# Performance work log

Measured on AMD Instinct MI355X. Metric: run time of the kernel, lower is better.

## Reference

```python
import jax, jax.numpy as jnp
import numpy as np
import math

B, SV, ST, D, H = 16, 1024, 512, 768, 8
DH = D // H


def layernorm(x, g, b, eps=1e-5):
    m = jnp.mean(x, axis=-1, keepdims=True)
    v = jnp.var(x, axis=-1, keepdims=True)
    return (x - m) / jnp.sqrt(v + eps) * g + b


def setup_inputs() -> dict:
    key = jax.random.key(0)
    ks = jax.random.split(key, 12)
    s = 1.0 / math.sqrt(D)
    inp = {
        "visual_features": jax.random.normal(ks[0], (B, SV, D), jnp.float32),
        "text_features": jax.random.normal(ks[1], (B, ST, D), jnp.float32),
        "visual_mask": jnp.ones((B, SV), jnp.int32),
        "text_mask": jnp.ones((B, ST), jnp.int32),
        "Wq": jax.random.normal(ks[2], (D, D), jnp.float32) * s,
        "bq": jnp.zeros((D,), jnp.float32),
        "Wk": jax.random.normal(ks[3], (D, D), jnp.float32) * s,
        "bk": jnp.zeros((D,), jnp.float32),
        "Wv": jax.random.normal(ks[4], (D, D), jnp.float32) * s,
        "bv": jnp.zeros((D,), jnp.float32),
        "Wo": jax.random.normal(ks[5], (D, D), jnp.float32) * s,
        "bo": jnp.zeros((D,), jnp.float32),
        "ln1_g": jnp.ones((D,), jnp.float32),
        "ln1_b": jnp.zeros((D,), jnp.float32),
        "Wf": jax.random.normal(ks[6], (2 * D, D), jnp.float32) * (1.0 / math.sqrt(2 * D)),
        "bf": jnp.zeros((D,), jnp.float32),
        "ln2_g": jnp.ones((D,), jnp.float32),
        "ln2_b": jnp.zeros((D,), jnp.float32),
    }
    return inp


def _heads(x):
    b, s, _ = x.shape
    return x.reshape(b, s, H, DH)


def _cross_attn(q_feats, kv_feats, kv_mask, Wq, bq, Wk, bk, Wv, bv):
    # q_feats: [B,Sq,D], kv_feats: [B,Sk,D], kv_mask: [B,Sk] or None
    q = _heads(q_feats @ Wq + bq)   # [B,Sq,H,DH]
    k = _heads(kv_feats @ Wk + bk)  # [B,Sk,H,DH]
    v = _heads(kv_feats @ Wv + bv)
    scores = jnp.einsum('bqhd,bkhd->bhqk', q, k) / math.sqrt(DH)
    if kv_mask is not None:
        scores = jnp.where(kv_mask[:, None, None, :] == 0, -jnp.inf, scores)
    attn = jax.nn.softmax(scores, axis=-1)  # dropout is identity in eval
    out = jnp.einsum('bhqk,bkhd->bqhd', attn, v)
    return out.reshape(q_feats.shape[0], q_feats.shape[1], D)


def reference(visual_features, text_features, visual_mask, text_mask,
              Wq, bq, Wk, bk, Wv, bv, Wo, bo, ln1_g, ln1_b,
              Wf, bf, ln2_g, ln2_b):
    # visual queries attend to text
    v2t = _cross_attn(visual_features, text_features, text_mask, Wq, bq, Wk, bk, Wv, bv)
    # text queries attend to visual
    t2v = _cross_attn(text_features, visual_features, visual_mask, Wq, bq, Wk, bk, Wv, bv)
    attended_visual = layernorm(visual_features + (v2t @ Wo + bo), ln1_g, ln1_b)
    attended_text = layernorm(text_features + (t2v @ Wo + bo), ln1_g, ln1_b)
    # masked mean pooling
    vm = visual_mask[:, :, None].astype(jnp.float32)
    pooled_v = (attended_visual * vm).sum(1) / vm.sum(1)
    tm = text_mask[:, :, None].astype(jnp.float32)
    pooled_t = (attended_text * tm).sum(1) / tm.sum(1)
    fused = jnp.concatenate([pooled_v, pooled_t], axis=-1) @ Wf + bf
    fused = layernorm(fused, ln2_g, ln2_b)  # dropout identity in eval
    return fused
```

## Files before the change

kernel.cpp:

```cpp
#include <hip/hip_runtime.h>

typedef __bf16 bf16x8 __attribute__((ext_vector_type(8)));
typedef float f32x4 __attribute__((ext_vector_type(4)));
typedef unsigned short u16;
typedef unsigned int u32;
typedef u16 u16x8 __attribute__((ext_vector_type(8)));
typedef u16 u16x4 __attribute__((ext_vector_type(4)));


__device__ __forceinline__ u16 f2bf(float f) {
    u32 u = __builtin_bit_cast(u32, f);
    u32 r = u + 0x7FFFu + ((u >> 16) & 1u);
    return (u16)(r >> 16);
}

__device__ __forceinline__ float bf2f(u16 b) {
    u32 u = ((u32)b) << 16;
    return __builtin_bit_cast(float, u);
}

__device__ __forceinline__ f32x4 mfma16(bf16x8 a, bf16x8 b, f32x4 c) {
    return __builtin_amdgcn_mfma_f32_16x16x32_bf16(a, b, c, 0, 0, 0);
}

#define GLOAD_LDS16(g, l) __builtin_amdgcn_global_load_lds( \
    (__attribute__((address_space(1))) void*)(g), \
    (__attribute__((address_space(3))) void*)(l), 16, 0, 0)


__global__ __launch_bounds__(256) void k_cvt_x(const float* __restrict__ vf,
                                               const float* __restrict__ tf,
                                               u16* __restrict__ X, int nvis4) {
    int i = blockIdx.x * 256 + threadIdx.x;
    f32x4 v = (i < nvis4) ? ((const f32x4*)vf)[i] : ((const f32x4*)tf)[i - nvis4];
    u16x4 o = { f2bf(v[0]), f2bf(v[1]), f2bf(v[2]), f2bf(v[3]) };
    ((u16x4*)X)[i] = o;
}

__global__ __launch_bounds__(256) void k_transpose(const float* __restrict__ src,
                                                   u16* __restrict__ dst,
                                                   int K0, int N0) {
    __shared__ float t[64][65];
    int ntx = N0 >> 6;
    int k0 = (blockIdx.x / ntx) << 6, n0 = (blockIdx.x % ntx) << 6;
    int c = threadIdx.x & 63, rr = threadIdx.x >> 6;
#pragma unroll
    for (int q = 0; q < 16; q++) {
        int r = q * 4 + rr;
        t[r][c] = src[(size_t)(k0 + r) * N0 + n0 + c];
    }
    __syncthreads();
#pragma unroll
    for (int q = 0; q < 16; q++) {
        int r = q * 4 + rr;
        dst[(size_t)(n0 + r) * K0 + k0 + c] = f2bf(t[c][r]);
    }
}

__global__ __launch_bounds__(256) void k_bias(const float* __restrict__ bq,
                                              const float* __restrict__ bk,
                                              const float* __restrict__ bv,
                                              float* __restrict__ bqkv) {
    int n = blockIdx.x * 256 + threadIdx.x;
    if (n < 2304) {
        const float* s = (n < 768) ? bq : ((n < 1536) ? bk : bv);
        int r = (n < 768) ? n : ((n < 1536) ? n - 768 : n - 1536);
        bqkv[n] = s[r];
    }
}

__global__ __launch_bounds__(256) void k_zero(float* __restrict__ p) {
    p[blockIdx.x * 256 + threadIdx.x] = 0.f;
}

template <bool OUT_BF16, bool ADD_RES, bool SPLIT_VT>
__global__ __launch_bounds__(256) void k_gemm(const u16* __restrict__ A,
                                              const u16* __restrict__ Bt,
                                              const float* __restrict__ bias,
                                              const float* __restrict__ resA,
                                              const float* __restrict__ resB,
                                              void* __restrict__ Cout,
                                              int Ndim, int Kdim, int mvisL,
                                              u16* __restrict__ VtGp, int Rtot) {
    __shared__ alignas(16) u16 sA[128 * 32];
    __shared__ alignas(16) u16 sB[128 * 32];
    const int tid = threadIdx.x, wid = tid >> 6, lane = tid & 63;
    const int nwg = gridDim.x;
    const int wg = (blockIdx.x & 7) * (nwg >> 3) + (blockIdx.x >> 3);
    const int ntiles = Ndim >> 7;
    const int mt = wg / ntiles, nt = wg - mt * ntiles;
    const int m0 = mt << 7, n0 = nt << 7;
    const int wm = wid >> 1, wn = wid & 1;
    f32x4 acc[4][4] = {};

    const int r0 = tid >> 2, p0 = tid & 3;
    const int r1 = 64 + (tid >> 2);
    const u16* ga0 = A + (size_t)(m0 + r0) * Kdim + p0 * 8;
    const u16* ga1 = A + (size_t)(m0 + r1) * Kdim + p0 * 8;
    const u16* gb0 = Bt + (size_t)(n0 + r0) * Kdim + p0 * 8;
    const u16* gb1 = Bt + (size_t)(n0 + r1) * Kdim + p0 * 8;
    u16* lA0 = sA + (wid * 64) * 8;
    u16* lA1 = sA + (256 + wid * 64) * 8;
    u16* lB0 = sB + (wid * 64) * 8;
    u16* lB1 = sB + (256 + wid * 64) * 8;

    const int arow = (wm << 6) + (lane & 15);
    const int brow = (wn << 6) + (lane & 15);
    const int kg = (lane >> 4) * 8;

    for (int kt = 0; kt < Kdim; kt += 32) {
        GLOAD_LDS16(ga0 + kt, lA0);
        GLOAD_LDS16(ga1 + kt, lA1);
        GLOAD_LDS16(gb0 + kt, lB0);
        GLOAD_LDS16(gb1 + kt, lB1);
        __syncthreads();
        bf16x8 av[4], bw[4];
#pragma unroll
        for (int i = 0; i < 4; i++) av[i] = *(const bf16x8*)&sA[(arow + i * 16) * 32 + kg];
#pragma unroll
        for (int j = 0; j < 4; j++) bw[j] = *(const bf16x8*)&sB[(brow + j * 16) * 32 + kg];
#pragma unroll
        for (int i = 0; i < 4; i++)
#pragma unroll
            for (int j = 0; j < 4; j++) acc[i][j] = mfma16(av[i], bw[j], acc[i][j]);
        __syncthreads();
    }

    const int col0 = n0 + (wn << 6) + (lane & 15);
    const int rowb = m0 + (wm << 6) + ((lane >> 4) << 2);
    float bvals[4];
#pragma unroll
    for (int j = 0; j < 4; j++) bvals[j] = bias[col0 + j * 16];

    if constexpr (SPLIT_VT) {
        if (n0 >= 1536) {
            const int vcol0 = col0 - 1536;
#pragma unroll
            for (int i = 0; i < 4; i++) {
#pragma unroll
                for (int j = 0; j < 4; j++) {
                    u16x4 o4;
#pragma unroll
                    for (int rg = 0; rg < 4; rg++) o4[rg] = f2bf(acc[i][j][rg] + bvals[j]);
                    *(u16x4*)&VtGp[(size_t)(vcol0 + j * 16) * Rtot + rowb + i * 16] = o4;
                }
            }
            return;
        }
    }

#pragma unroll
    for (int i = 0; i < 4; i++) {
#pragma unroll
        for (int rg = 0; rg < 4; rg++) {
            const int row = rowb + i * 16 + rg;
            const float* rp = nullptr;
            if constexpr (ADD_RES)
                rp = (row < mvisL) ? resA + (size_t)row * 768
                                   : resB + (size_t)(row - mvisL) * 768;
#pragma unroll
            for (int j = 0; j < 4; j++) {
                const int col = col0 + j * 16;
                float v = acc[i][j][rg] + bvals[j];
                if constexpr (ADD_RES) v += rp[col];
                if constexpr (OUT_BF16)
                    ((u16*)Cout)[(size_t)row * Ndim + col] = f2bf(v);
                else
                    ((float*)Cout)[(size_t)row * Ndim + col] = v;
            }
        }
    }
}

__global__ __launch_bounds__(512) void k_attn(const u16* __restrict__ qkv,
                                              const u16* __restrict__ VtG,
                                              const int* __restrict__ vmaskc,
                                              const int* __restrict__ tmaskc,
                                              u16* __restrict__ attn, int CHn, int Rtot) {
    __shared__ alignas(16) u16 Kl[2][128 * 128];
    __shared__ alignas(16) u16 Vt[2][96 * 128];
    __shared__ alignas(16) u16 Pl[8][16 * 128];
    __shared__ float mk[2][128];

    const int bx = blockIdx.x;
    int b, h, qbase, kbase, nqt, ntl;
    const int* mask;
    const int vcap = CHn * 8;
    if (bx < vcap) {
        b = bx >> 3; h = bx & 7;
        qbase = b << 10; kbase = (CHn << 10) + (b << 9);
        mask = tmaskc + (b << 9); nqt = 4; ntl = 2;
    } else {
        const int bx2 = bx - vcap;
        b = bx2 >> 3; h = bx2 & 7;
        qbase = (CHn << 10) + (b << 9); kbase = b << 10;
        mask = vmaskc + (b << 10); nqt = 2; ntl = 3;
    }
    const int ntile = 1 << ntl;
    const int nsteps = nqt << ntl;
    const int tid = threadIdx.x, wid = tid >> 6, lane = tid & 63;
    const int l15 = lane & 15, l4 = lane >> 4;
    const float scale = 0.10206207261596577f;

    int koff[4];
#pragma unroll
    for (int kk = 0; kk < 4; kk++) koff[kk] = ((kk * 4 + l4) ^ (l15 & 7)) << 3;

    auto kt_of = [&](int s) {
        const int qt = s >> ntl, ktr = s & (ntile - 1);
        return (qt & 1) ? (ntile - 1 - ktr) : ktr;
    };
    auto stage = [&](int kt, int pb) {
#pragma unroll
        for (int it = 0; it < 4; ++it) {
            const int cb = it * 512 + (wid << 6);
            const int c = cb + lane;
            const int r = c >> 4, s8 = c & 15;
            const int k8 = s8 ^ (r & 7);
            const u16* src = qkv + (size_t)(kbase + (kt << 7) + r) * 2304 + 768 + h * 96
                             + (k8 < 12 ? k8 * 8 : 0);
            GLOAD_LDS16(src, &Kl[pb][(size_t)cb * 8]);
        }
#pragma unroll
        for (int it = 0; it < 3; ++it) {
            const int cb = it * 512 + (wid << 6);
            const int c = cb + lane;
            const int d = c >> 4, s8 = c & 15;
            const int k8 = s8 ^ (d & 7);
            const u16* src = VtG + (size_t)(h * 96 + d) * Rtot + kbase + (kt << 7) + k8 * 8;
            GLOAD_LDS16(src, &Vt[pb][(size_t)cb * 8]);
        }
        if (tid < 128) mk[pb][tid] = mask[(kt << 7) + tid] ? 0.f : -1e30f;
    };

    stage(kt_of(0), 0);
    int s = 0;
    for (int qt = 0; qt < nqt; ++qt) {
        bf16x8 aq[2][3];
#pragma unroll
        for (int qs = 0; qs < 2; ++qs) {
            const int qr = qbase + (qt << 8) + (wid << 5) + qs * 16 + l15;
#pragma unroll
            for (int kk = 0; kk < 3; kk++) {
                bf16x8 tq = *(const bf16x8*)&qkv[(size_t)qr * 2304 + h * 96 + kk * 32 + l4 * 8];
#pragma unroll
                for (int e = 0; e < 8; e++) tq[e] = (__bf16)((float)tq[e] * scale);
                aq[qs][kk] = tq;
            }
        }
        f32x4 o[2][6] = {};
        float mrun[2][4], lrun[2][4];
#pragma unroll
        for (int qs = 0; qs < 2; ++qs)
#pragma unroll
            for (int rg = 0; rg < 4; rg++) { mrun[qs][rg] = -1e30f; lrun[qs][rg] = 0.f; }

        for (int ktr = 0; ktr < ntile; ++ktr, ++s) {
            const int cur = s & 1;
            __syncthreads();
            if (s + 1 < nsteps) stage(kt_of(s + 1), cur ^ 1);

            f32x4 sc[2][8];
#pragma unroll
            for (int j = 0; j < 8; j++) {
                const int rbase = (j * 16 + l15) * 128;
                bf16x8 bk[3];
#pragma unroll
                for (int kk = 0; kk < 3; kk++)
                    bk[kk] = *(const bf16x8*)&Kl[cur][rbase + koff[kk]];
#pragma unroll
                for (int qs = 0; qs < 2; ++qs) {
                    f32x4 cj = {0.f, 0.f, 0.f, 0.f};
#pragma unroll
                    for (int kk = 0; kk < 3; kk++) cj = mfma16(aq[qs][kk], bk[kk], cj);
                    sc[qs][j] = cj;
                }
            }

#pragma unroll
            for (int qs = 0; qs < 2; ++qs) {
                float tmax[4] = {-1e30f, -1e30f, -1e30f, -1e30f};
#pragma unroll
                for (int j = 0; j < 8; j++) {
                    float mb = mk[cur][j * 16 + l15];
#pragma unroll
                    for (int rg = 0; rg < 4; rg++) {
                        float v = sc[qs][j][rg] + mb;
                        sc[qs][j][rg] = v;
                        tmax[rg] = fmaxf(tmax[rg], v);
                    }
                }
#pragma unroll
                for (int d = 1; d < 16; d <<= 1)
#pragma unroll
                    for (int rg = 0; rg < 4; rg++)
                        tmax[rg] = fmaxf(tmax[rg], __shfl_xor(tmax[rg], d));
                int need = 0;
#pragma unroll
                for (int rg = 0; rg < 4; rg++) need |= (tmax[rg] > mrun[qs][rg] + 8.f) ? 1 : 0;
                if (__any(need)) {
#pragma unroll
                    for (int rg = 0; rg < 4; rg++) {
                        float mn = fmaxf(mrun[qs][rg], tmax[rg]);
                        float corr = __expf(mrun[qs][rg] - mn);
                        mrun[qs][rg] = mn;
                        lrun[qs][rg] *= corr;
#pragma unroll
                        for (int j6 = 0; j6 < 6; j6++) o[qs][j6][rg] *= corr;
                    }
                }
                float tsum[4] = {0.f, 0.f, 0.f, 0.f};
#pragma unroll
                for (int j = 0; j < 8; j++)
#pragma unroll
                    for (int rg = 0; rg < 4; rg++) {
                        float p = __expf(sc[qs][j][rg] - mrun[qs][rg]);
                        tsum[rg] += p;
                        const int prow = l4 * 4 + rg;
                        Pl[wid][prow * 128 + ((j * 16 + l15) ^ ((prow & 7) << 3))] = f2bf(p);
                    }
#pragma unroll
                for (int d = 1; d < 16; d <<= 1)
#pragma unroll
                    for (int rg = 0; rg < 4; rg++) tsum[rg] += __shfl_xor(tsum[rg], d);
#pragma unroll
                for (int rg = 0; rg < 4; rg++) lrun[qs][rg] += tsum[rg];

#pragma unroll
                for (int kk = 0; kk < 4; kk++) {
                    bf16x8 ap = *(const bf16x8*)&Pl[wid][l15 * 128 + koff[kk]];
#pragma unroll
                    for (int j6 = 0; j6 < 6; j6++) {
                        bf16x8 bv8 = *(const bf16x8*)&Vt[cur][(j6 * 16 + l15) * 128 + koff[kk]];
                        o[qs][j6] = mfma16(ap, bv8, o[qs][j6]);
                    }
                }
            }
        }

#pragma unroll
        for (int qs = 0; qs < 2; ++qs) {
            float inv[4];
#pragma unroll
            for (int rg = 0; rg < 4; rg++) inv[rg] = 1.f / lrun[qs][rg];
            const size_t orow = (size_t)(qbase + (qt << 8) + (wid << 5) + qs * 16);
#pragma unroll
            for (int j6 = 0; j6 < 6; j6++)
#pragma unroll
                for (int rg = 0; rg < 4; rg++)
                    attn[(orow + l4 * 4 + rg) * 768 + h * 96 + j6 * 16 + l15] =
                        f2bf(o[qs][j6][rg] * inv[rg]);
        }
    }
}

__global__ __launch_bounds__(256) void k_ln_pool(const u16* __restrict__ X,
                                                 const int* __restrict__ vmaskc,
                                                 const int* __restrict__ tmaskc,
                                                 const float* __restrict__ g,
                                                 const float* __restrict__ bb,
                                                 float* __restrict__ pooled,
                                                 int mvisL, int bg0) {
    __shared__ float pool[768];
    const int tid = threadIdx.x, wid = tid >> 6, lane = tid & 63;
    const int row0 = blockIdx.x << 5;
    const bool vis = row0 < mvisL;
    const int* mask = vis ? vmaskc : tmaskc;
    const int mbase = vis ? 0 : mvisL;
    const int bl = vis ? (row0 >> 10) : ((row0 - mvisL) >> 9);
    float* pout = pooled + (vis ? 0 : 12288) + (size_t)(bg0 + bl) * 768;

    float gv[12], bv2[12];
#pragma unroll
    for (int k = 0; k < 12; k++) { gv[k] = g[lane + k * 64]; bv2[k] = bb[lane + k * 64]; }
    float acc[12] = {};
    for (int rr = 0; rr < 8; ++rr) {
        const int row = row0 + (wid << 3) + rr;
        const u16* x = X + (size_t)row * 768;
        float xs[12], sm = 0.f, s2 = 0.f;
#pragma unroll
        for (int k = 0; k < 12; k++) {
            float tv = bf2f(x[lane + k * 64]);
            xs[k] = tv; sm += tv; s2 += tv * tv;
        }
#pragma unroll
        for (int d = 1; d < 64; d <<= 1) { sm += __shfl_xor(sm, d); s2 += __shfl_xor(s2, d); }
        const float mean = sm * (1.f / 768.f);
        const float rstd = rsqrtf(s2 * (1.f / 768.f) - mean * mean + 1e-5f);
        const float mv = (float)mask[row - mbase];
#pragma unroll
        for (int k = 0; k < 12; k++) acc[k] += ((xs[k] - mean) * rstd * gv[k] + bv2[k]) * mv;
    }
    pool[tid] = 0.f; pool[tid + 256] = 0.f; pool[tid + 512] = 0.f;
    __syncthreads();
#pragma unroll
    for (int k = 0; k < 12; k++) atomicAdd(&pool[lane + k * 64], acc[k]);
    __syncthreads();
    atomicAdd(&pout[tid], pool[tid]);
    atomicAdd(&pout[tid + 256], pool[tid + 256]);
    atomicAdd(&pout[tid + 512], pool[tid + 512]);
}

__device__ __forceinline__ float blk_sum(float v, volatile float* tmp) {
#pragma unroll
    for (int d = 1; d < 64; d <<= 1) v += __shfl_xor(v, d);
    __syncthreads();
    if ((threadIdx.x & 63) == 0) tmp[threadIdx.x >> 6] = v;
    __syncthreads();
    return tmp[0] + tmp[1] + tmp[2] + tmp[3];
}

__global__ __launch_bounds__(256) void k_final(const float* __restrict__ pooled,
                                               const int* __restrict__ vmask,
                                               const int* __restrict__ tmask,
                                               const float* __restrict__ Wf,
                                               const float* __restrict__ bfv,
                                               const float* __restrict__ g2,
                                               const float* __restrict__ b2,
                                               float* __restrict__ out) {
    __shared__ float sh[1536];
    __shared__ float red[4];
    const int b = blockIdx.x, tid = threadIdx.x;
    float cv = 0.f, ct = 0.f;
    for (int i = tid; i < 1024; i += 256) cv += (float)vmask[(b << 10) + i];
    for (int i = tid; i < 512; i += 256) ct += (float)tmask[(b << 9) + i];
    cv = blk_sum(cv, red);
    ct = blk_sum(ct, red);
    const float iv = 1.f / cv, itv = 1.f / ct;
#pragma unroll
    for (int k = 0; k < 3; k++) {
        int j = tid + (k << 8);
        sh[j] = pooled[b * 768 + j] * iv;
        sh[768 + j] = pooled[12288 + b * 768 + j] * itv;
    }
    __syncthreads();
    float f0 = bfv[tid], f1 = bfv[tid + 256], f2 = bfv[tid + 512];
    for (int i = 0; i < 1536; i++) {
        const float pv = sh[i];
        const float* w = Wf + (size_t)i * 768;
        f0 += pv * w[tid];
        f1 += pv * w[tid + 256];
        f2 += pv * w[tid + 512];
    }
    float sm = blk_sum(f0 + f1 + f2, red);
    float s2 = blk_sum(f0 * f0 + f1 * f1 + f2 * f2, red);
    const float mean = sm * (1.f / 768.f);
    const float rstd = rsqrtf(s2 * (1.f / 768.f) - mean * mean + 1e-5f);
    out[b * 768 + tid] = (f0 - mean) * rstd * g2[tid] + b2[tid];
    out[b * 768 + tid + 256] = (f1 - mean) * rstd * g2[tid + 256] + b2[tid + 256];
    out[b * 768 + tid + 512] = (f2 - mean) * rstd * g2[tid + 512] + b2[tid + 512];
}

extern "C" void kernel_launch(void* const* d_in, const int* in_sizes, int n_in,
                              void* d_out, int out_size, void* d_ws, size_t ws_size,
                              hipStream_t stream) {
    (void)in_sizes; (void)n_in; (void)out_size;
    const float* vf = (const float*)d_in[0];
    const float* tf = (const float*)d_in[1];
    const int* vmask = (const int*)d_in[2];
    const int* tmask = (const int*)d_in[3];
    const float* Wq = (const float*)d_in[4];
    const float* bq = (const float*)d_in[5];
    const float* Wk = (const float*)d_in[6];
    const float* bk = (const float*)d_in[7];
    const float* Wv = (const float*)d_in[8];
    const float* bv = (const float*)d_in[9];
    const float* Wo = (const float*)d_in[10];
    const float* bo = (const float*)d_in[11];
    const float* g1 = (const float*)d_in[12];
    const float* b1 = (const float*)d_in[13];
    const float* Wf = (const float*)d_in[14];
    const float* bfv = (const float*)d_in[15];
    const float* g2 = (const float*)d_in[16];
    const float* b2 = (const float*)d_in[17];
    float* outp = (float*)d_out;

    int CH = 16;
    while (CH > 1 && 4826112ull + (size_t)CH * 11796480ull > ws_size) CH >>= 1;
    const int NC = 16 / CH;
    const int Rtot = CH * 1536;

    char* ws = (char*)d_ws;
    u16*   wsW      = (u16*)(ws);
    u16*   wsWo     = (u16*)(ws + 3538944);
    float* wsBqkv   = (float*)(ws + 4718592);
    float* wsPooled = (float*)(ws + 4727808);
    u16*   wsX      = (u16*)(ws + 4826112);
    char*  qkvBase  = ws + 4826112 + (size_t)CH * 2359296;
    u16*   wsQKV    = (u16*)qkvBase;
    u16*   wsOproj  = (u16*)qkvBase;
    u16*   wsVtG    = (u16*)(qkvBase + (size_t)CH * 7077888);
    u16*   wsAttn   = wsX;

    k_transpose<<<dim3(144), dim3(256), 0, stream>>>(Wq, wsW, 768, 768);
    k_transpose<<<dim3(144), dim3(256), 0, stream>>>(Wk, wsW + 589824, 768, 768);
    k_transpose<<<dim3(144), dim3(256), 0, stream>>>(Wv, wsW + 1179648, 768, 768);
    k_transpose<<<dim3(144), dim3(256), 0, stream>>>(Wo, wsWo, 768, 768);
    k_bias<<<dim3(9), dim3(256), 0, stream>>>(bq, bk, bv, wsBqkv);
    k_zero<<<dim3(96), dim3(256), 0, stream>>>(wsPooled);

    for (int c = 0; c < NC; ++c) {
        const float* vfc = vf + (size_t)c * CH * 1024 * 768;
        const float* tfc = tf + (size_t)c * CH * 512 * 768;
        const int* vmc = vmask + c * CH * 1024;
        const int* tmc = tmask + c * CH * 512;

        k_cvt_x<<<dim3(CH * 1152), dim3(256), 0, stream>>>(vfc, tfc, wsX, CH * 196608);

        k_gemm<true, false, true><<<dim3(CH * 216), dim3(256), 0, stream>>>(
            wsX, wsW, wsBqkv, nullptr, nullptr, (void*)wsQKV, 2304, 768, 0, wsVtG, Rtot);

        k_attn<<<dim3(CH * 16), dim3(512), 0, stream>>>(
            wsQKV, wsVtG, vmc, tmc, wsAttn, CH, Rtot);

        k_gemm<true, true, false><<<dim3(CH * 72), dim3(256), 0, stream>>>(
            wsAttn, wsWo, bo, vfc, tfc, (void*)wsOproj, 768, 768, CH * 1024, nullptr, 0);

        k_ln_pool<<<dim3(CH * 48), dim3(256), 0, stream>>>(
            wsOproj, vmc, tmc, g1, b1, wsPooled, CH * 1024, c * CH);
    }

    k_final<<<dim3(16), dim3(256), 0, stream>>>(wsPooled, vmask, tmask, Wf, bfv, g2, b2, outp);
}
```

Baseline: 446.8 us.

## Double-buffer LDS tiles in GEMM to overlap global loads with MFMA

The GEMM kernel gets two LDS buffers for the A and B tiles. It prefetches the next K-slice into the alternate buffer right after the barrier, then runs the MFMAs on the current buffer. This removes the second barrier per iteration and hides global-to-LDS load latency behind compute. The cost is twice the shared memory per workgroup, which may reduce occupancy.

```diff
diff --git a/kernel.cpp b/kernel.cpp
--- a/kernel.cpp
+++ b/kernel.cpp
@@ -82,8 +82,8 @@
                                               void* __restrict__ Cout,
                                               int Ndim, int Kdim, int mvisL,
                                               u16* __restrict__ VtGp, int Rtot) {
-    __shared__ alignas(16) u16 sA[128 * 32];
-    __shared__ alignas(16) u16 sB[128 * 32];
+    __shared__ alignas(16) u16 sA[2][128 * 32];
+    __shared__ alignas(16) u16 sB[2][128 * 32];
     const int tid = threadIdx.x, wid = tid >> 6, lane = tid & 63;
     const int nwg = gridDim.x;
     const int wg = (blockIdx.x & 7) * (nwg >> 3) + (blockIdx.x >> 3);
@@ -94,36 +94,40 @@
     f32x4 acc[4][4] = {};
 
     const int r0 = tid >> 2, p0 = tid & 3;
-    const int r1 = 64 + (tid >> 2);
+    const int r1 = 64 + r0;
     const u16* ga0 = A + (size_t)(m0 + r0) * Kdim + p0 * 8;
     const u16* ga1 = A + (size_t)(m0 + r1) * Kdim + p0 * 8;
     const u16* gb0 = Bt + (size_t)(n0 + r0) * Kdim + p0 * 8;
     const u16* gb1 = Bt + (size_t)(n0 + r1) * Kdim + p0 * 8;
-    u16* lA0 = sA + (wid * 64) * 8;
-    u16* lA1 = sA + (256 + wid * 64) * 8;
-    u16* lB0 = sB + (wid * 64) * 8;
-    u16* lB1 = sB + (256 + wid * 64) * 8;
+    const int loff0 = wid * 512;
+    const int loff1 = 2048 + wid * 512;
 
     const int arow = (wm << 6) + (lane & 15);
     const int brow = (wn << 6) + (lane & 15);
     const int kg = (lane >> 4) * 8;
 
-    for (int kt = 0; kt < Kdim; kt += 32) {
-        GLOAD_LDS16(ga0 + kt, lA0);
-        GLOAD_LDS16(ga1 + kt, lA1);
-        GLOAD_LDS16(gb0 + kt, lB0);
-        GLOAD_LDS16(gb1 + kt, lB1);
+    auto stage = [&](int kt, int pb) {
+        GLOAD_LDS16(ga0 + kt, &sA[pb][loff0]);
+        GLOAD_LDS16(ga1 + kt, &sA[pb][loff1]);
+        GLOAD_LDS16(gb0 + kt, &sB[pb][loff0]);
+        GLOAD_LDS16(gb1 + kt, &sB[pb][loff1]);
+    };
+
+    const int niter = Kdim >> 5;
+    stage(0, 0);
+    for (int it = 0; it < niter; ++it) {
+        const int cur = it & 1;
         __syncthreads();
+        if (it + 1 < niter) stage((it + 1) << 5, cur ^ 1);
         bf16x8 av[4], bw[4];
 #pragma unroll
-        for (int i = 0; i < 4; i++) av[i] = *(const bf16x8*)&sA[(arow + i * 16) * 32 + kg];
-#pragma unroll
-        for (int j = 0; j < 4; j++) bw[j] = *(const bf16x8*)&sB[(brow + j * 16) * 32 + kg];
+        for (int i = 0; i < 4; i++) av[i] = *(const bf16x8*)&sA[cur][(arow + i * 16) * 32 + kg];
+#pragma unroll
+        for (int j = 0; j < 4; j++) bw[j] = *(const bf16x8*)&sB[cur][(brow + j * 16) * 32 + kg];
 #pragma unroll
         for (int i = 0; i < 4; i++)
 #pragma unroll
             for (int j = 0; j < 4; j++) acc[i][j] = mfma16(av[i], bw[j], acc[i][j]);
-        __syncthreads();
     }
 
     const int col0 = n0 + (wn << 6) + (lane & 15);
```

New measurement: 457.1 us, median of 2. +2.3%, slower.
